# Optimization experiments

Hardware: AMD Instinct MI355X
Metric: run time of the kernel (lower is better)

The kernel has to match this reference:

```python
import jax, jax.numpy as jnp
import numpy as np

APERTURE = 256
IGNORE_ITSELF = False
FMAX = jnp.float32(3.4028235e38)  # tf.float32.max


def setup_inputs() -> dict:
    key = jax.random.key(0)
    ks = jax.random.split(key, 5)
    n, m, d = 4096, 1024, 1024
    scale = 1.0 / np.sqrt(m)
    x = jax.random.normal(ks[0], (n, m), dtype=jnp.float32)
    WK = jax.random.normal(ks[1], (m, d), dtype=jnp.float32) * scale
    WQ = jax.random.normal(ks[2], (m, d), dtype=jnp.float32) * scale
    WV = jax.random.normal(ks[3], (m, d), dtype=jnp.float32) * scale
    Wout = jax.random.normal(ks[4], (d, m), dtype=jnp.float32) * scale
    return {"x": x, "WK": WK, "WQ": WQ, "WV": WV, "Wout": Wout}


def reference(x, WK, WQ, WV, Wout):
    n = x.shape[0]
    K = x @ WK                      # [n, d]
    Q = (x @ WQ) * 0.06             # [n, d]
    V = x @ WV                      # [n, d]
    logits = Q @ K.T                # [n, n]

    i = jnp.arange(n)[:, None]
    j = jnp.arange(n)[None, :]
    if IGNORE_ITSELF:
        keep = (i != j).astype(jnp.float32)
        logits = logits * keep - FMAX * (1.0 - keep)
    if APERTURE > 0:
        # tf: mask = 1 - band_part(ones, -aperture, aperture); negative num_lower
        # keeps the whole lower triangle, so mask==1 exactly where j - i > aperture.
        keep = (j - i > APERTURE).astype(jnp.float32)
        logits = logits * keep - FMAX * (1.0 - keep)

    att_weights = jax.nn.softmax(logits, axis=-1)  # [n, n]
    # dropout is identity (training=False). NOTE faithful quirk: transpose_a=True.
    y = att_weights.T @ V           # [n, d]
    y = y @ Wout                    # [n, m]
    return (y, att_weights)
```

## Files before the change

### kernel.cpp

```cpp
#include <hip/hip_runtime.h>
#include <cstdint>
#include <cstddef>

#define N_TOK 4096
#define M_DIM 1024
#define APER  256
#define UNIF_START 3839

typedef __attribute__((ext_vector_type(8))) short short8;
typedef __attribute__((ext_vector_type(4))) float float4_t;

__device__ __forceinline__ unsigned short f2bf(float x) {
    union { float f; uint32_t u; } v; v.f = x;
    uint32_t u = v.u;
    u += 0x7FFFu + ((u >> 16) & 1u);
    return (unsigned short)(u >> 16);
}

__device__ __forceinline__ void gload16(const void* g, void* l) {
    __builtin_amdgcn_global_load_lds(
        (const __attribute__((address_space(1))) void*)g,
        (__attribute__((address_space(3))) void*)l, 16, 0, 0);
}

__global__ __launch_bounds__(256) void cast_bf16(const float* __restrict__ src,
                                                 unsigned short* __restrict__ dst, int n) {
    const int i = (blockIdx.x * 256 + threadIdx.x) * 4;
    if (i >= n) return;
    const float4 v = *reinterpret_cast<const float4*>(&src[i]);
    ushort4 o;
    o.x = f2bf(v.x); o.y = f2bf(v.y); o.z = f2bf(v.z); o.w = f2bf(v.w);
    *reinterpret_cast<ushort4*>(&dst[i]) = o;
}

__global__ __launch_bounds__(256) void wtrans3(const float* __restrict__ W0, const float* __restrict__ W1,
                                               const float* __restrict__ W2,
                                               unsigned short* __restrict__ D0, unsigned short* __restrict__ D1,
                                               unsigned short* __restrict__ D2) {
    const int z = blockIdx.z;
    const float* src = z == 0 ? W0 : (z == 1 ? W1 : W2);
    unsigned short* dst = z == 0 ? D0 : (z == 1 ? D1 : D2);
    __shared__ unsigned short tile[32][33];
    const int c0 = blockIdx.x * 32, r0 = blockIdx.y * 32;
    const int tx = threadIdx.x & 31, ty = threadIdx.x >> 5;
#pragma unroll
    for (int i = ty; i < 32; i += 8)
        tile[i][tx] = f2bf(src[(size_t)(r0 + i) * M_DIM + c0 + tx]);
    __syncthreads();
#pragma unroll
    for (int i = ty; i < 32; i += 8)
        dst[(size_t)(c0 + i) * M_DIM + r0 + tx] = tile[tx][i];
}

__global__ __launch_bounds__(256) void transpose_bf16(const unsigned short* __restrict__ src,
                                                      unsigned short* __restrict__ dst,
                                                      int R, int C) {
    __shared__ unsigned short tile[32][33];
    const int c0 = blockIdx.x * 32, r0 = blockIdx.y * 32;
    const int tx = threadIdx.x & 31, ty = threadIdx.x >> 5;
#pragma unroll
    for (int i = ty; i < 32; i += 8)
        tile[i][tx] = src[(size_t)(r0 + i) * C + c0 + tx];
    __syncthreads();
#pragma unroll
    for (int i = ty; i < 32; i += 8)
        dst[(size_t)(c0 + i) * R + r0 + tx] = tile[tx][i];
}

template <int SKIP>
__global__ __launch_bounds__(256) void nt64sq(const unsigned short* __restrict__ A,
                                              const unsigned short* __restrict__ B,
                                              float* __restrict__ Cf,
                                              unsigned short* __restrict__ Cb,
                                              int N, int K) {
    const int by   = (SKIP == 1) ? ((int)gridDim.y - 1 - (int)blockIdx.y) : (int)blockIdx.y;
    const int row0 = by * 64;
    const int col0 = blockIdx.x * 64;

    __shared__ unsigned short Asb[64 * 32];
    __shared__ unsigned short Bsb[64 * 32];

    const int t = threadIdx.x, w = t >> 6, lane = t & 63;
    float4_t acc[4] = {};

    const int sr   = lane >> 2;
    const int sk   = ((lane & 3) ^ ((sr >> 1) & 3)) * 8;
    const int m    = lane & 15;
    const int slot = ((lane >> 4) ^ ((m >> 1) & 3)) * 8;

    for (int k0 = 0; k0 < K; k0 += 32) {
        if (SKIP == 1) {
            if ((k0 > row0 + 63 - APER - 1) && (k0 + 31 < UNIF_START)) continue;
        }
        const int rr = w * 16 + sr;
        gload16(&A[(size_t)(row0 + rr) * K + k0 + sk], &Asb[w * 512]);
        gload16(&B[(size_t)(col0 + rr) * K + k0 + sk], &Bsb[w * 512]);
        __syncthreads();
        const short8 af = *reinterpret_cast<const short8*>(&Asb[(w * 16 + m) * 32 + slot]);
        short8 bf[4];
#pragma unroll
        for (int j = 0; j < 4; ++j)
            bf[j] = *reinterpret_cast<const short8*>(&Bsb[(j * 16 + m) * 32 + slot]);
#pragma unroll
        for (int j = 0; j < 4; ++j)
            acc[j] = __builtin_amdgcn_mfma_f32_16x16x32_bf16(af, bf[j], acc[j], 0, 0, 0);
        __syncthreads();
    }

    const int crow = row0 + w * 16 + (lane >> 4) * 4;
    const int ccol = col0 + m;
#pragma unroll
    for (int j = 0; j < 4; ++j)
#pragma unroll
        for (int r = 0; r < 4; ++r) {
            const float v = acc[j][r];
            const size_t idx = (size_t)(crow + r) * N + ccol + j * 16;
            if (Cf) Cf[idx] = v;
            if (Cb) Cb[idx] = f2bf(v);
        }
}

__global__ __launch_bounds__(256) void atv_db(const unsigned short* __restrict__ A,
                                              const unsigned short* __restrict__ B,
                                              float* __restrict__ C) {
    const int byr  = (int)blockIdx.y;
    const int by   = (byr & 1) ? (63 - (byr >> 1)) : (byr >> 1);
    const int row0 = by * 64;
    const int col0 = blockIdx.x * 128;

    __shared__ unsigned short As[2][64 * 64];
    __shared__ unsigned short Bs[2][128 * 64];

    const int t = threadIdx.x, w = t >> 6, lane = t & 63;
    const int wr = (w >> 1) * 32, wc = (w & 1) * 64;
    const int q = lane >> 4, m = lane & 15;

    const int srow = lane >> 3;
    const int schk = ((lane & 7) ^ (srow & 7)) * 8;

    int aoff[2][2], boff[4][2];
#pragma unroll
    for (int i = 0; i < 2; ++i)
#pragma unroll
        for (int h = 0; h < 2; ++h)
            aoff[i][h] = (wr + i * 16 + m) * 64 + (((h * 4 + q) ^ (m & 7)) * 8);
#pragma unroll
    for (int j = 0; j < 4; ++j)
#pragma unroll
        for (int h = 0; h < 2; ++h)
            boff[j][h] = (wc + j * 16 + m) * 64 + (((h * 4 + q) ^ (m & 7)) * 8);

    const int limit = row0 - 194;
    int nPre = (limit >= 0) ? (limit / 64 + 1) : 0;
    if (nPre > 59) nPre = 59;
    const int nT = nPre + 5;

    float4_t acc[2][4] = {};

    auto kof = [&](int s) { return s < nPre ? s * 64 : 3776 + (s - nPre) * 64; };

    auto stage = [&](int buf, int k0) {
#pragma unroll
        for (int c = 0; c < 2; ++c) {
            const int r0 = w * 16 + c * 8;
            gload16(&A[(size_t)(row0 + r0 + srow) * (size_t)N_TOK + k0 + schk],
                    &As[buf][r0 * 64]);
        }
#pragma unroll
        for (int c = 0; c < 4; ++c) {
            const int r0 = w * 32 + c * 8;
            gload16(&B[(size_t)(col0 + r0 + srow) * (size_t)N_TOK + k0 + schk],
                    &Bs[buf][r0 * 64]);
        }
    };

    stage(0, kof(0));
    __syncthreads();

    int cur = 0;
    for (int s = 0; s < nT; ++s) {
        if (s + 1 < nT) stage(cur ^ 1, kof(s + 1));
        short8 af[2][2], bf[4][2];
#pragma unroll
        for (int i = 0; i < 2; ++i)
#pragma unroll
            for (int h = 0; h < 2; ++h)
                af[i][h] = *reinterpret_cast<const short8*>(&As[cur][aoff[i][h]]);
#pragma unroll
        for (int j = 0; j < 4; ++j)
#pragma unroll
            for (int h = 0; h < 2; ++h)
                bf[j][h] = *reinterpret_cast<const short8*>(&Bs[cur][boff[j][h]]);
#pragma unroll
        for (int i = 0; i < 2; ++i)
#pragma unroll
            for (int j = 0; j < 4; ++j)
#pragma unroll
                for (int h = 0; h < 2; ++h)
                    acc[i][j] = __builtin_amdgcn_mfma_f32_16x16x32_bf16(af[i][h], bf[j][h],
                                                                        acc[i][j], 0, 0, 0);
        __syncthreads();
        cur ^= 1;
    }

#pragma unroll
    for (int i = 0; i < 2; ++i)
#pragma unroll
        for (int j = 0; j < 4; ++j)
#pragma unroll
            for (int r = 0; r < 4; ++r)
                C[(size_t)(row0 + wr + i * 16 + q * 4 + r) * M_DIM + col0 + wc + j * 16 + m] =
                    acc[i][j][r];
}

__global__ __launch_bounds__(256) void logits_db(const unsigned short* __restrict__ A,
                                                 const unsigned short* __restrict__ B,
                                                 float* __restrict__ att,
                                                 float* __restrict__ rowsum) {
    int rem = (int)blockIdx.x, y = 0;
    for (;;) {
        const int c = 30 - (y >> 1);
        if (rem < c) break;
        rem -= c; ++y;
    }
    const int row0 = y * 64;
    const int col0 = ((y >> 1) + 2 + rem) * 128;

    __shared__ unsigned short As[2][64 * 64];
    __shared__ unsigned short Bs[2][128 * 64];

    const int t = threadIdx.x, w = t >> 6, lane = t & 63;
    const int wr = (w >> 1) * 32, wc = (w & 1) * 64;
    const int q = lane >> 4, m = lane & 15;

    const int srow = lane >> 3;
    const int schk = ((lane & 7) ^ (srow & 7)) * 8;

    int aoff[2][2], boff[4][2];
#pragma unroll
    for (int i = 0; i < 2; ++i)
#pragma unroll
        for (int h = 0; h < 2; ++h)
            aoff[i][h] = (wr + i * 16 + m) * 64 + (((h * 4 + q) ^ (m & 7)) * 8);
#pragma unroll
    for (int j = 0; j < 4; ++j)
#pragma unroll
        for (int h = 0; h < 2; ++h)
            boff[j][h] = (wc + j * 16 + m) * 64 + (((h * 4 + q) ^ (m & 7)) * 8);

    float4_t acc[2][4] = {};

    auto stage = [&](int buf, int k0) {
#pragma unroll
        for (int c = 0; c < 2; ++c) {
            const int r0 = w * 16 + c * 8;
            gload16(&A[(size_t)(row0 + r0 + srow) * M_DIM + k0 + schk], &As[buf][r0 * 64]);
        }
#pragma unroll
        for (int c = 0; c < 4; ++c) {
            const int r0 = w * 32 + c * 8;
            gload16(&B[(size_t)(col0 + r0 + srow) * M_DIM + k0 + schk], &Bs[buf][r0 * 64]);
        }
    };

    stage(0, 0);
    __syncthreads();

    int cur = 0;
    for (int s = 0; s < 16; ++s) {
        if (s + 1 < 16) stage(cur ^ 1, (s + 1) * 64);
        short8 af[2][2], bf[4][2];
#pragma unroll
        for (int i = 0; i < 2; ++i)
#pragma unroll
            for (int h = 0; h < 2; ++h)
                af[i][h] = *reinterpret_cast<const short8*>(&As[cur][aoff[i][h]]);
#pragma unroll
        for (int j = 0; j < 4; ++j)
#pragma unroll
            for (int h = 0; h < 2; ++h)
                bf[j][h] = *reinterpret_cast<const short8*>(&Bs[cur][boff[j][h]]);
#pragma unroll
        for (int i = 0; i < 2; ++i)
#pragma unroll
            for (int j = 0; j < 4; ++j)
#pragma unroll
                for (int h = 0; h < 2; ++h)
                    acc[i][j] = __builtin_amdgcn_mfma_f32_16x16x32_bf16(af[i][h], bf[j][h],
                                                                        acc[i][j], 0, 0, 0);
        __syncthreads();
        cur ^= 1;
    }

#pragma unroll
    for (int i = 0; i < 2; ++i) {
#pragma unroll
        for (int r = 0; r < 4; ++r) {
            const int gr = row0 + wr + i * 16 + q * 4 + r;
            float partial = 0.0f;
#pragma unroll
            for (int j = 0; j < 4; ++j) {
                const int gc = col0 + wc + j * 16 + m;
                float val;
                if (gr >= UNIF_START) {
                    val = 1.0f;
                } else if (gc > gr + APER) {
                    val = __expf(acc[i][j][r]);
                    partial += val;
                } else {
                    val = 0.0f;
                }
                att[(size_t)gr * N_TOK + gc] = val;
            }
            partial += __shfl_xor(partial, 1, 64);
            partial += __shfl_xor(partial, 2, 64);
            partial += __shfl_xor(partial, 4, 64);
            partial += __shfl_xor(partial, 8, 64);
            if (m == 0 && gr < UNIF_START) atomicAdd(&rowsum[gr], partial);
        }
    }
}

__global__ __launch_bounds__(256) void mfma_qkv(const unsigned short* __restrict__ xb,
                                                const unsigned short* __restrict__ WKt,
                                                const unsigned short* __restrict__ WQt,
                                                const unsigned short* __restrict__ WVWt,
                                                unsigned short* __restrict__ Kb,
                                                unsigned short* __restrict__ Qb,
                                                unsigned short* __restrict__ VWb) {
    const int row0  = blockIdx.y * 128;
    const int col0g = blockIdx.x * 128;
    const int seg   = col0g >> 10;
    const int col0  = col0g & 1023;
    const unsigned short* B = seg == 0 ? WKt : (seg == 1 ? WQt : WVWt);
    unsigned short*       C = seg == 0 ? Kb  : (seg == 1 ? Qb  : VWb);
    const float alpha = (seg == 1) ? 0.06f : 1.0f;

    __shared__ unsigned short Asb[128 * 32];
    __shared__ unsigned short Bsb[128 * 32];

    const int t = threadIdx.x, w = t >> 6, lane = t & 63;
    const int wr = (w >> 1) * 64, wc = (w & 1) * 64;

    float4_t acc[4][4] = {};

    const int sr   = lane >> 2;
    const int sk   = ((lane & 3) ^ ((sr >> 1) & 3)) * 8;
    const int m    = lane & 15;
    const int slot = ((lane >> 4) ^ ((m >> 1) & 3)) * 8;

    for (int k0 = 0; k0 < M_DIM; k0 += 32) {
#pragma unroll
        for (int cc = 0; cc < 2; ++cc) {
            const int c = 2 * w + cc;
            const int rr = c * 16 + sr;
            gload16(&xb[(size_t)(row0 + rr) * M_DIM + k0 + sk], &Asb[c * 512]);
            gload16(&B[(size_t)(col0 + rr) * M_DIM + k0 + sk], &Bsb[c * 512]);
        }
        __syncthreads();
        short8 af[4], bf[4];
#pragma unroll
        for (int i = 0; i < 4; ++i)
            af[i] = *reinterpret_cast<const short8*>(&Asb[(wr + i * 16 + m) * 32 + slot]);
#pragma unroll
        for (int j = 0; j < 4; ++j)
            bf[j] = *reinterpret_cast<const short8*>(&Bsb[(wc + j * 16 + m) * 32 + slot]);
#pragma unroll
        for (int i = 0; i < 4; ++i)
#pragma unroll
            for (int j = 0; j < 4; ++j)
                acc[i][j] = __builtin_amdgcn_mfma_f32_16x16x32_bf16(af[i], bf[j], acc[i][j], 0, 0, 0);
        __syncthreads();
    }

    const int crow = row0 + wr + (lane >> 4) * 4;
    const int ccol = col0 + wc + m;
#pragma unroll
    for (int i = 0; i < 4; ++i)
#pragma unroll
        for (int j = 0; j < 4; ++j)
#pragma unroll
            for (int r = 0; r < 4; ++r)
                C[(size_t)(crow + i * 16 + r) * M_DIM + ccol + j * 16] = f2bf(alpha * acc[i][j][r]);
}

__global__ __launch_bounds__(256) void init_rowsum(float* __restrict__ rowsum) {
    const int i = blockIdx.x * 256 + threadIdx.x;
    if (i < N_TOK) rowsum[i] = (i >= UNIF_START) ? (float)N_TOK : 0.0f;
}

__global__ __launch_bounds__(256) void finalize_att(float* __restrict__ att,
                                                    unsigned short* __restrict__ attT,
                                                    const float* __restrict__ rowsum) {
    const int j0 = blockIdx.x * 64, i0 = blockIdx.y * 64;
    const int t = threadIdx.x;
    const int rl = t >> 4;
    const int c4 = (t & 15) * 4;
    const float u = 1.0f / (float)N_TOK;

    if (j0 + 63 <= i0 + APER) {
#pragma unroll
        for (int s = 0; s < 4; ++s) {
            const int i = i0 + rl + 16 * s;
            const float val = (i >= UNIF_START) ? u : 0.0f;
            float4 v; v.x = v.y = v.z = v.w = val;
            *reinterpret_cast<float4*>(&att[(size_t)i * N_TOK + j0 + c4]) = v;
        }
        const unsigned short bu = f2bf(u);
#pragma unroll
        for (int s = 0; s < 4; ++s) {
            const int j = j0 + rl + 16 * s;
            ushort4 o;
            o.x = (i0 + c4 + 0 >= UNIF_START) ? bu : 0;
            o.y = (i0 + c4 + 1 >= UNIF_START) ? bu : 0;
            o.z = (i0 + c4 + 2 >= UNIF_START) ? bu : 0;
            o.w = (i0 + c4 + 3 >= UNIF_START) ? bu : 0;
            *reinterpret_cast<ushort4*>(&attT[(size_t)j * N_TOK + i0 + c4]) = o;
        }
        return;
    }

    __shared__ unsigned short tile[64][72];
#pragma unroll
    for (int s = 0; s < 4; ++s) {
        const int il = rl + 16 * s;
        const int i  = i0 + il;
        const float inv = 1.0f / rowsum[i];
        float4 v = *reinterpret_cast<const float4*>(&att[(size_t)i * N_TOK + j0 + c4]);
        v.x *= inv; v.y *= inv; v.z *= inv; v.w *= inv;
        *reinterpret_cast<float4*>(&att[(size_t)i * N_TOK + j0 + c4]) = v;
        ushort4 b;
        b.x = f2bf(v.x); b.y = f2bf(v.y); b.z = f2bf(v.z); b.w = f2bf(v.w);
        *reinterpret_cast<ushort4*>(&tile[il][c4]) = b;
    }
    __syncthreads();
#pragma unroll
    for (int s = 0; s < 4; ++s) {
        const int jl = rl + 16 * s;
        ushort4 o;
        o.x = tile[c4 + 0][jl];
        o.y = tile[c4 + 1][jl];
        o.z = tile[c4 + 2][jl];
        o.w = tile[c4 + 3][jl];
        *reinterpret_cast<ushort4*>(&attT[(size_t)(j0 + jl) * N_TOK + i0 + c4]) = o;
    }
}

extern "C" void kernel_launch(void* const* d_in, const int* in_sizes, int n_in,
                              void* d_out, int out_size, void* d_ws, size_t ws_size,
                              hipStream_t stream) {
    const float* x    = (const float*)d_in[0];
    const float* WK   = (const float*)d_in[1];
    const float* WQ   = (const float*)d_in[2];
    const float* WV   = (const float*)d_in[3];
    const float* Wout = (const float*)d_in[4];

    float* y   = (float*)d_out;
    float* att = y + (size_t)N_TOK * M_DIM;

    unsigned short* base = (unsigned short*)d_ws;
    const size_t MEG = 1u << 20;
    unsigned short* xb    = base;
    unsigned short* WKt   = base + 4  * MEG;
    unsigned short* WQt   = base + 5  * MEG;
    unsigned short* Woutt = base + 6  * MEG;
    unsigned short* WVb   = base + 7  * MEG;
    unsigned short* WVWt  = base + 8  * MEG;
    unsigned short* Kb    = base + 9  * MEG;
    unsigned short* Qb    = base + 13 * MEG;
    unsigned short* VWb   = base + 17 * MEG;
    unsigned short* attT  = base + 4  * MEG;
    float*          rowsum = (float*)(base + 20 * MEG);
    unsigned short* VWt   = xb;

    const dim3 blk(256);

    cast_bf16<<<dim3((N_TOK * M_DIM) / 1024), blk, 0, stream>>>(x, xb, N_TOK * M_DIM);
    cast_bf16<<<dim3((M_DIM * M_DIM) / 1024), blk, 0, stream>>>(WV, WVb, M_DIM * M_DIM);
    wtrans3<<<dim3(M_DIM / 32, M_DIM / 32, 3), blk, 0, stream>>>(WK, WQ, Wout, WKt, WQt, Woutt);

    nt64sq<0><<<dim3(M_DIM / 64, M_DIM / 64), blk, 0, stream>>>(Woutt, WVb, nullptr, WVWt,
                                                                M_DIM, M_DIM);

    mfma_qkv<<<dim3(24, N_TOK / 128), blk, 0, stream>>>(xb, WKt, WQt, WVWt, Kb, Qb, VWb);

    transpose_bf16<<<dim3(M_DIM / 32, N_TOK / 32), blk, 0, stream>>>(VWb, VWt, N_TOK, M_DIM);

    init_rowsum<<<dim3(N_TOK / 256), blk, 0, stream>>>(rowsum);
    logits_db<<<dim3(930), blk, 0, stream>>>(Qb, Kb, att, rowsum);

    finalize_att<<<dim3(N_TOK / 64, N_TOK / 64), blk, 0, stream>>>(att, attT, rowsum);

    atv_db<<<dim3(M_DIM / 128, N_TOK / 64), blk, 0, stream>>>(attT, VWt, y);
}
```

Before: 284.2 us.

## Fold uniform-row contribution into a rank-1 init and split-K the attention-value GEMM

Rows at and beyond the uniform-softmax start all have weight 1/N, so their contribution to y is a per-column average of the tail of VW. That average is now computed once and broadcast into y as an initial value, and those rows are zeroed in attT. The att^T·V GEMM then covers only the strictly nonzero prefix K-range. Longer row blocks are split into two K-halves across blocks and accumulated into y with atomicAdd, which balances the triangular work. The cost is two small extra kernels, float atomics on y that make summation order nondeterministic, and the broadcast being computed from bf16 VW values.

```diff
diff --git a/kernel.cpp b/kernel.cpp
--- a/kernel.cpp
+++ b/kernel.cpp
@@ -15,6 +15,11 @@
     uint32_t u = v.u;
     u += 0x7FFFu + ((u >> 16) & 1u);
     return (unsigned short)(u >> 16);
+}
+
+__device__ __forceinline__ float bf2f(unsigned short b) {
+    union { uint32_t u; float f; } v; v.u = ((uint32_t)b) << 16;
+    return v.f;
 }
 
 __device__ __forceinline__ void gload16(const void* g, void* l) {
@@ -73,7 +78,7 @@
                                               float* __restrict__ Cf,
                                               unsigned short* __restrict__ Cb,
                                               int N, int K) {
-    const int by   = (SKIP == 1) ? ((int)gridDim.y - 1 - (int)blockIdx.y) : (int)blockIdx.y;
+    const int by   = (int)blockIdx.y;
     const int row0 = by * 64;
     const int col0 = blockIdx.x * 64;
 
@@ -89,9 +94,6 @@
     const int slot = ((lane >> 4) ^ ((m >> 1) & 3)) * 8;
 
     for (int k0 = 0; k0 < K; k0 += 32) {
-        if (SKIP == 1) {
-            if ((k0 > row0 + 63 - APER - 1) && (k0 + 31 < UNIF_START)) continue;
-        }
         const int rr = w * 16 + sr;
         gload16(&A[(size_t)(row0 + rr) * K + k0 + sk], &Asb[w * 512]);
         gload16(&B[(size_t)(col0 + rr) * K + k0 + sk], &Bsb[w * 512]);
@@ -120,13 +122,42 @@
         }
 }
 
-__global__ __launch_bounds__(256) void atv_db(const unsigned short* __restrict__ A,
-                                              const unsigned short* __restrict__ B,
-                                              float* __restrict__ C) {
-    const int byr  = (int)blockIdx.y;
-    const int by   = (byr & 1) ? (63 - (byr >> 1)) : (byr >> 1);
+__global__ __launch_bounds__(256) void sum_vw_tail(const unsigned short* __restrict__ VWb,
+                                                   float* __restrict__ s) {
+    const int c = blockIdx.x * 256 + threadIdx.x;
+    float acc = 0.0f;
+    for (int i = UNIF_START; i < N_TOK; ++i)
+        acc += bf2f(VWb[(size_t)i * M_DIM + c]);
+    s[c] = acc * (1.0f / (float)N_TOK);
+}
+
+__global__ __launch_bounds__(256) void init_y(float* __restrict__ y, const float* __restrict__ s) {
+    const float4 sv = reinterpret_cast<const float4*>(s)[threadIdx.x];
+    const int r0 = blockIdx.x * 4;
+#pragma unroll
+    for (int r = 0; r < 4; ++r)
+        reinterpret_cast<float4*>(&y[(size_t)(r0 + r) * M_DIM])[threadIdx.x] = sv;
+}
+
+__global__ __launch_bounds__(256) void atv_split(const unsigned short* __restrict__ A,
+                                                 const unsigned short* __restrict__ B,
+                                                 float* __restrict__ y) {
+    const int bid  = (int)blockIdx.x;
+    const int x    = bid & 7;
+    const int unit = bid >> 3;
+    int by, s0, ns;
+    if (unit < 32) {
+        by = 4 + unit; s0 = 0; ns = by - 3;
+    } else {
+        const int v = unit - 32;
+        by = 36 + (v >> 1);
+        const int tot = by - 3;
+        const int n1  = (tot + 1) >> 1;
+        if (v & 1) { s0 = n1; ns = tot - n1; }
+        else       { s0 = 0;  ns = n1; }
+    }
     const int row0 = by * 64;
-    const int col0 = blockIdx.x * 128;
+    const int col0 = x * 128;
 
     __shared__ unsigned short As[2][64 * 64];
     __shared__ unsigned short Bs[2][128 * 64];
@@ -150,16 +181,10 @@
         for (int h = 0; h < 2; ++h)
             boff[j][h] = (wc + j * 16 + m) * 64 + (((h * 4 + q) ^ (m & 7)) * 8);
 
-    const int limit = row0 - 194;
-    int nPre = (limit >= 0) ? (limit / 64 + 1) : 0;
-    if (nPre > 59) nPre = 59;
-    const int nT = nPre + 5;
-
     float4_t acc[2][4] = {};
 
-    auto kof = [&](int s) { return s < nPre ? s * 64 : 3776 + (s - nPre) * 64; };
-
-    auto stage = [&](int buf, int k0) {
+    auto stage = [&](int buf, int s) {
+        const int k0 = (s0 + s) * 64;
 #pragma unroll
         for (int c = 0; c < 2; ++c) {
             const int r0 = w * 16 + c * 8;
@@ -174,12 +199,12 @@
         }
     };
 
-    stage(0, kof(0));
+    stage(0, 0);
     __syncthreads();
 
     int cur = 0;
-    for (int s = 0; s < nT; ++s) {
-        if (s + 1 < nT) stage(cur ^ 1, kof(s + 1));
+    for (int s = 0; s < ns; ++s) {
+        if (s + 1 < ns) stage(cur ^ 1, s + 1);
         short8 af[2][2], bf[4][2];
 #pragma unroll
         for (int i = 0; i < 2; ++i)
@@ -209,8 +234,9 @@
         for (int j = 0; j < 4; ++j)
 #pragma unroll
             for (int r = 0; r < 4; ++r)
-                C[(size_t)(row0 + wr + i * 16 + q * 4 + r) * M_DIM + col0 + wc + j * 16 + m] =
-                    acc[i][j][r];
+                atomicAdd(&y[(size_t)(row0 + wr + i * 16 + q * 4 + r) * M_DIM +
+                             col0 + wc + j * 16 + m],
+                          acc[i][j][r]);
 }
 
 __global__ __launch_bounds__(256) void logits_db(const unsigned short* __restrict__ A,
@@ -406,16 +432,11 @@
             float4 v; v.x = v.y = v.z = v.w = val;
             *reinterpret_cast<float4*>(&att[(size_t)i * N_TOK + j0 + c4]) = v;
         }
-        const unsigned short bu = f2bf(u);
+        const ushort4 z = {0, 0, 0, 0};
 #pragma unroll
         for (int s = 0; s < 4; ++s) {
             const int j = j0 + rl + 16 * s;
-            ushort4 o;
-            o.x = (i0 + c4 + 0 >= UNIF_START) ? bu : 0;
-            o.y = (i0 + c4 + 1 >= UNIF_START) ? bu : 0;
-            o.z = (i0 + c4 + 2 >= UNIF_START) ? bu : 0;
-            o.w = (i0 + c4 + 3 >= UNIF_START) ? bu : 0;
-            *reinterpret_cast<ushort4*>(&attT[(size_t)j * N_TOK + i0 + c4]) = o;
+            *reinterpret_cast<ushort4*>(&attT[(size_t)j * N_TOK + i0 + c4]) = z;
         }
         return;
     }
@@ -430,7 +451,11 @@
         v.x *= inv; v.y *= inv; v.z *= inv; v.w *= inv;
         *reinterpret_cast<float4*>(&att[(size_t)i * N_TOK + j0 + c4]) = v;
         ushort4 b;
-        b.x = f2bf(v.x); b.y = f2bf(v.y); b.z = f2bf(v.z); b.w = f2bf(v.w);
+        if (i >= UNIF_START) {
+            b.x = b.y = b.z = b.w = 0;
+        } else {
+            b.x = f2bf(v.x); b.y = f2bf(v.y); b.z = f2bf(v.z); b.w = f2bf(v.w);
+        }
         *reinterpret_cast<ushort4*>(&tile[il][c4]) = b;
     }
     __syncthreads();
@@ -471,6 +496,7 @@
     unsigned short* VWb   = base + 17 * MEG;
     unsigned short* attT  = base + 4  * MEG;
     float*          rowsum = (float*)(base + 20 * MEG);
+    float*          svec   = (float*)(base + 20 * MEG) + 4096;
     unsigned short* VWt   = xb;
 
     const dim3 blk(256);
@@ -485,11 +511,13 @@
     mfma_qkv<<<dim3(24, N_TOK / 128), blk, 0, stream>>>(xb, WKt, WQt, WVWt, Kb, Qb, VWb);
 
     transpose_bf16<<<dim3(M_DIM / 32, N_TOK / 32), blk, 0, stream>>>(VWb, VWt, N_TOK, M_DIM);
+    sum_vw_tail<<<dim3(M_DIM / 256), blk, 0, stream>>>(VWb, svec);
+    init_y<<<dim3(N_TOK / 4), blk, 0, stream>>>(y, svec);
 
     init_rowsum<<<dim3(N_TOK / 256), blk, 0, stream>>>(rowsum);
     logits_db<<<dim3(930), blk, 0, stream>>>(Qb, Kb, att, rowsum);
 
     finalize_att<<<dim3(N_TOK / 64, N_TOK / 64), blk, 0, stream>>>(att, attT, rowsum);
 
-    atv_db<<<dim3(M_DIM / 128, N_TOK / 64), blk, 0, stream>>>(attT, VWt, y);
-}
+    atv_split<<<dim3(704), blk, 0, stream>>>(attT, VWt, y);
+}
```

After: 285.3 us. Within noise of the previous version (+0.4%).
